# Kernel tuning notes

Measured on AMD Instinct MI355X. Metric: run time of the kernel, lower is better.

Reference implementation:

```python
import math
import jax, jax.numpy as jnp
import numpy as np

NUM_HEADS = 16
HEAD_DIM = 128
BLOCK = 256
EPS = 1e-6


def _get_slopes(n):
    def p2(n):
        start = 2 ** (-2 ** (-(math.log2(n) - 3)))
        return [start * start ** i for i in range(n)]
    if math.log2(n).is_integer():
        return p2(n)
    c = 2 ** math.floor(math.log2(n))
    return p2(c) + _get_slopes(2 * c)[0::2][: n - c]


def setup_inputs() -> dict:
    key = jax.random.key(0)
    ks = jax.random.split(key, 4)
    d_in, d_out = 2048, 2048
    x = jax.random.normal(ks[0], (2, 4096, d_in), dtype=jnp.float32)
    Wqkv = jax.random.normal(ks[1], (d_in, 3 * NUM_HEADS * HEAD_DIM), dtype=jnp.float32) * 0.02
    Wg = jax.random.normal(ks[2], (d_in, NUM_HEADS * HEAD_DIM), dtype=jnp.float32) * 0.02
    Wout = jax.random.normal(ks[3], (NUM_HEADS * HEAD_DIM, d_out), dtype=jnp.float32) * 0.02
    norm_w = jnp.ones((NUM_HEADS * HEAD_DIM,), dtype=jnp.float32)
    return {"x": x, "Wqkv": Wqkv, "Wg": Wg, "Wout": Wout, "norm_w": norm_w}


def reference(x, Wqkv, Wg, Wout, norm_w):
    b, n, _ = x.shape
    h, d = NUM_HEADS, HEAD_DIM
    nb = n // BLOCK  # seq_len chosen divisible by block_size

    # slopes (ALiBi-style), shape [h,1,1]
    slope = jnp.asarray(_get_slopes(h), dtype=jnp.float32).reshape(h, 1, 1)

    qkv = jax.nn.silu(x @ Wqkv)                       # [b,n,3hd]
    qkv = qkv.reshape(b, n, h, 3 * d)
    q, k, v = jnp.split(qkv, 3, axis=-1)              # each [b,n,h,d]
    q = q.transpose(0, 2, 1, 3)                       # [b,h,n,d]
    k = k.transpose(0, 2, 1, 3)
    v = v.transpose(0, 2, 1, 3)

    # per-position decay factors within a block
    arr = jnp.arange(BLOCK, dtype=jnp.float32) + 1.0          # [B]
    q_decay = jnp.exp(-slope * arr[:, None])                  # [h,B,1]
    k_decay = jnp.exp(-slope * (BLOCK - arr[:, None]))        # [h,B,1]
    idx = arr[:, None] - arr[None, :]                         # [B,B]
    diag_decay = jnp.where(idx >= 0, jnp.exp(-slope[None] * idx[None, None]), 0.0)  # [1,h,B,B]
    block_decay = jnp.exp(-slope * BLOCK)                     # [h,1,1]

    # blocked xs: [nb, b, h, B, d]
    def to_blocks(t):
        return t.reshape(b, h, nb, BLOCK, d).transpose(2, 0, 1, 3, 4)

    qb, kb, vb = to_blocks(q), to_blocks(k), to_blocks(v)

    def step(kv, blk):
        qi, ki, vi = blk                                       # [b,h,B,d]
        # inter-block: (qi * q_decay) @ kv  -> [b,h,B,d]
        non_diag = jnp.einsum('bhmd,bhde->bhme', qi * q_decay, kv)
        # intra-block causal decayed attention
        qk = jnp.einsum('bhmd,bhnd->bhmn', qi, ki) * diag_decay
        diag = jnp.einsum('bhmn,bhne->bhme', qk, vi)
        out = non_diag + diag
        kv_new = block_decay * kv + jnp.einsum('bhmd,bhme->bhde', ki * k_decay, vi)
        return kv_new, out

    kv0 = jnp.zeros((b, h, d, d), dtype=jnp.float32)
    _, out_blocks = jax.lax.scan(step, kv0, (qb, kb, vb))      # [nb,b,h,B,d]
    o = out_blocks.transpose(1, 2, 0, 3, 4).reshape(b, h, n, d)
    o = o.transpose(0, 2, 1, 3).reshape(b, n, h * d)           # [b,n,hd]

    # T5 (RMS) LayerNorm
    var = jnp.mean(o * o, axis=-1, keepdims=True)
    o = o * jax.lax.rsqrt(var + EPS) * norm_w

    # output gate and projection
    o = jax.nn.sigmoid(x @ Wg) * o
    return o @ Wout
```

## Files before the change

### kernel.cpp

```cpp
#include <hip/hip_runtime.h>
#include <cstddef>

typedef float f32x4 __attribute__((ext_vector_type(4)));
typedef __bf16 bf16x8 __attribute__((ext_vector_type(8)));
typedef unsigned short u16x8 __attribute__((ext_vector_type(8)));
typedef unsigned short u16x4 __attribute__((ext_vector_type(4)));

constexpr int NB = 2, S = 4096, H = 16, D = 128;
constexpr int DIN = 2048, NQKV = 6144, HD = 2048;
constexpr int BLK = 256, NBL = 16;

constexpr size_t SZ_XB    = (size_t)NB * S * DIN * 2;
constexpr size_t SZ_WQKVT = (size_t)NQKV * DIN * 2;
constexpr size_t SZ_WGT   = (size_t)HD * DIN * 2;
constexpr size_t SZ_WOUTT = (size_t)HD * HD * 2;
constexpr size_t SZ_QKVB  = (size_t)NB * S * NQKV * 2;
constexpr size_t SZ_GB    = (size_t)NB * S * HD * 2;
constexpr size_t SZ_ST    = (size_t)NB * H * NBL * D * D * 2;
constexpr size_t SZ_OB    = (size_t)NB * S * HD * 2;

__device__ __forceinline__ float bf2f(unsigned short u) {
  return __uint_as_float(((unsigned)u) << 16);
}
__device__ __forceinline__ unsigned short f2bf(float f) {
  unsigned u = __float_as_uint(f);
  u += 0x7fffu + ((u >> 16) & 1u);
  return (unsigned short)(u >> 16);
}
__device__ __forceinline__ void gload16(const void* g, void* l) {
  __builtin_amdgcn_global_load_lds(
      (const __attribute__((address_space(1))) unsigned int*)g,
      (__attribute__((address_space(3))) unsigned int*)l, 16, 0, 0);
}

__global__ __launch_bounds__(256) void cvt_bf16(
    const float* __restrict__ in, unsigned short* __restrict__ out) {
  const size_t id = (size_t)blockIdx.x * 256 + threadIdx.x;
  const float4 a = *(const float4*)&in[id * 8];
  const float4 c = *(const float4*)&in[id * 8 + 4];
  u16x8 o;
  o[0] = f2bf(a.x); o[1] = f2bf(a.y); o[2] = f2bf(a.z); o[3] = f2bf(a.w);
  o[4] = f2bf(c.x); o[5] = f2bf(c.y); o[6] = f2bf(c.z); o[7] = f2bf(c.w);
  *(u16x8*)&out[id * 8] = o;
}

__global__ __launch_bounds__(256) void transpose_cvt(
    const float* __restrict__ W, unsigned short* __restrict__ Wt, int K, int N) {
  __shared__ unsigned short tile[32][33];
  const int n0 = blockIdx.x * 32, k0 = blockIdx.y * 32;
  const int t = threadIdx.x;
  const int r = t >> 3, c4 = (t & 7) * 4;
  const float4 v = *(const float4*)&W[(size_t)(k0 + r) * N + n0 + c4];
  tile[r][c4 + 0] = f2bf(v.x);
  tile[r][c4 + 1] = f2bf(v.y);
  tile[r][c4 + 2] = f2bf(v.z);
  tile[r][c4 + 3] = f2bf(v.w);
  __syncthreads();
  u16x4 o;
  #pragma unroll
  for (int i = 0; i < 4; ++i) o[i] = tile[c4 + i][r];
  *(u16x4*)&Wt[(size_t)(n0 + r) * K + k0 + c4] = o;
}

template<int ACT>
__global__ __launch_bounds__(256, 3) void gemm128(
    const unsigned short* __restrict__ A, const unsigned short* __restrict__ Bt,
    void* __restrict__ O1, void* __restrict__ O2,
    int M, int N, int K, int NSPLIT) {
  __shared__ unsigned short lds[16384];
  char* ldsb = (char*)lds;
  const int t = threadIdx.x;
  const int lane = t & 63, wave = t >> 6;
  const int wr = wave >> 1, wc = wave & 1;
  const int l15 = lane & 15;

  const int nbm = M >> 7;
  const int nbmx = nbm >> 3;
  const int xcd = blockIdx.x & 7, q = blockIdx.x >> 3;
  const int bm = xcd * nbmx + (q % nbmx);
  const int bn = q / nbmx;

  const int cg = (t & 7) ^ ((t >> 3) & 7);
  const unsigned short* sA = A  + (size_t)(bm * 128 + (t >> 3)) * K + cg * 8;
  const unsigned short* sB = Bt + (size_t)(bn * 128 + (t >> 3)) * K + cg * 8;
  const int dstb = t << 4;

  int offA[2][4], offB[2][4];
  #pragma unroll
  for (int kk = 0; kk < 2; ++kk) {
    #pragma unroll
    for (int m = 0; m < 4; ++m) {
      const int row = wr * 64 + m * 16 + l15;
      offA[kk][m] = row * 128 + (((kk * 4 + (lane >> 4)) ^ (row & 7)) << 4);
    }
    #pragma unroll
    for (int n = 0; n < 4; ++n) {
      const int row = wc * 64 + n * 16 + l15;
      offB[kk][n] = 16384 + row * 128 + (((kk * 4 + (lane >> 4)) ^ (row & 7)) << 4);
    }
  }

  const int NT = K >> 6;
  f32x4 acc[4][4] = {};
  for (int u = 0; u < NT; ++u) {
    __syncthreads();
    const int ko = u * 64;
    #pragma unroll
    for (int i = 0; i < 4; ++i) {
      gload16(sA + (size_t)(i * 32) * K + ko, ldsb + i * 4096 + dstb);
      gload16(sB + (size_t)(i * 32) * K + ko, ldsb + 16384 + i * 4096 + dstb);
    }
    asm volatile("s_waitcnt vmcnt(0)" ::: "memory");
    __syncthreads();
    #pragma unroll
    for (int kk = 0; kk < 2; ++kk) {
      bf16x8 af[4], bfr[4];
      #pragma unroll
      for (int m = 0; m < 4; ++m) af[m] = *(const bf16x8*)(ldsb + offA[kk][m]);
      #pragma unroll
      for (int n = 0; n < 4; ++n) bfr[n] = *(const bf16x8*)(ldsb + offB[kk][n]);
      #pragma unroll
      for (int m = 0; m < 4; ++m)
        #pragma unroll
        for (int n = 0; n < 4; ++n)
          acc[m][n] = __builtin_amdgcn_mfma_f32_16x16x32_bf16(af[m], bfr[n], acc[m][n], 0, 0, 0);
    }
  }

  const int ro = (lane >> 4) * 4, co = l15;
  const bool lo = (bn * 128) < NSPLIT;
  #pragma unroll
  for (int m = 0; m < 4; ++m)
    #pragma unroll
    for (int n = 0; n < 4; ++n) {
      const int gc = bn * 128 + wc * 64 + n * 16 + co;
      #pragma unroll
      for (int r = 0; r < 4; ++r) {
        const int gr = bm * 128 + wr * 64 + m * 16 + ro + r;
        float v = acc[m][n][r];
        if constexpr (ACT == 0) {
          ((float*)O1)[(size_t)gr * N + gc] = v;
        } else {
          if (lo) {
            v = v / (1.f + __expf(-v));
            ((unsigned short*)O1)[(size_t)gr * NSPLIT + gc] = f2bf(v);
          } else {
            v = 1.f / (1.f + __expf(-v));
            ((unsigned short*)O2)[(size_t)gr * (N - NSPLIT) + (gc - NSPLIT)] = f2bf(v);
          }
        }
      }
    }
}

__global__ __launch_bounds__(256) void kv_outer(
    const unsigned short* __restrict__ qkv, unsigned short* __restrict__ st) {
  const int gid = blockIdx.x;
  const int j = gid & 15;
  const int bh = gid >> 4;
  const int h = bh & 15;
  const int b = bh >> 4;
  const float slope = exp2f(-0.5f * (float)(h + 1));
  const int t = threadIdx.x;
  __shared__ unsigned short kl[64][136];
  __shared__ unsigned short vl[64][136];
  float acc[8][8] = {};
  const int e0 = (t >> 4) * 8, f0 = (t & 15) * 8;
  for (int ch = 0; ch < 4; ++ch) {
    if (ch) __syncthreads();
    #pragma unroll
    for (int i = 0; i < 4; ++i) {
      const int cc = t + 256 * i;
      const int r = cc >> 4, c0 = (cc & 15) * 8;
      const int mb = ch * 64 + r;
      const int seq = b * S + j * BLK + mb;
      const u16x8 k8 = *(const u16x8*)&qkv[(size_t)seq * NQKV + h * 384 + 128 + c0];
      const float kd = expf(-slope * (float)(255 - mb));
      u16x8 kw;
      #pragma unroll
      for (int q2 = 0; q2 < 8; ++q2) kw[q2] = f2bf(bf2f(k8[q2]) * kd);
      *(u16x8*)&kl[r][c0] = kw;
      *(u16x8*)&vl[r][c0] = *(const u16x8*)&qkv[(size_t)seq * NQKV + h * 384 + 256 + c0];
    }
    __syncthreads();
    for (int m = 0; m < 64; ++m) {
      const u16x8 k8 = *(const u16x8*)&kl[m][e0];
      const u16x8 v8 = *(const u16x8*)&vl[m][f0];
      float kf[8], vf[8];
      #pragma unroll
      for (int q2 = 0; q2 < 8; ++q2) { kf[q2] = bf2f(k8[q2]); vf[q2] = bf2f(v8[q2]); }
      #pragma unroll
      for (int i = 0; i < 8; ++i)
        #pragma unroll
        for (int q2 = 0; q2 < 8; ++q2) acc[i][q2] += kf[i] * vf[q2];
    }
  }
  const size_t base = (size_t)gid * (D * D);
  #pragma unroll
  for (int q2 = 0; q2 < 8; ++q2) {
    u16x8 ow;
    #pragma unroll
    for (int i = 0; i < 8; ++i) ow[i] = f2bf(acc[i][q2]);
    *(u16x8*)&st[base + (size_t)(f0 + q2) * D + e0] = ow;
  }
}

__global__ __launch_bounds__(256) void kv_scan(unsigned short* __restrict__ st) {
  const int id = blockIdx.x * 256 + threadIdx.x;
  const int ef = id & (D * D - 1);
  const int bh = id >> 14;
  const int h = bh & 15;
  const float slope = exp2f(-0.5f * (float)(h + 1));
  const float bd = expf(-slope * 256.f);
  unsigned short* p = st + (size_t)bh * NBL * D * D + ef;
  float cur = 0.f;
  #pragma unroll
  for (int jj = 0; jj < NBL; ++jj) {
    const float m = bf2f(p[(size_t)jj * D * D]);
    p[(size_t)jj * D * D] = f2bf(cur);
    cur = bd * cur + m;
  }
}

__global__ __launch_bounds__(256) void attn_mfma(
    const unsigned short* __restrict__ qkv, const unsigned short* __restrict__ st,
    unsigned short* __restrict__ ob) {
  const int gid = blockIdx.x;
  const int half = gid & 1;
  const int rest = gid >> 1;
  const int j = rest & 15;
  const int bh = rest >> 4;
  const int h = bh & 15;
  const int b = bh >> 4;
  const float slope = exp2f(-0.5f * (float)(h + 1));
  const int t = threadIdx.x;
  const int lane = t & 63, wave = t >> 6, wr = wave >> 1, wc = wave & 1;

  __shared__ unsigned short ql[128][136];
  __shared__ unsigned short cb[128][136];
  __shared__ unsigned short pl[128][136];

  {
    const int r = t >> 4, c0 = (t & 15) * 8;
    const size_t stbase = (size_t)rest * (D * D);
    #pragma unroll
    for (int p = 0; p < 8; ++p) {
      const int seq = b * S + j * BLK + half * 128 + r + p * 16;
      *(u16x8*)&ql[r + p * 16][c0] = *(const u16x8*)&qkv[(size_t)seq * NQKV + h * 384 + c0];
      *(u16x8*)&cb[r + p * 16][c0] = *(const u16x8*)&st[stbase + (size_t)(r + p * 16) * D + c0];
    }
  }
  __syncthreads();

  f32x4 acc[4][4] = {};
  #pragma unroll
  for (int kk = 0; kk < 4; ++kk) {
    bf16x8 af[4], bfr[4];
    #pragma unroll
    for (int m = 0; m < 4; ++m)
      af[m] = *(const bf16x8*)&ql[wr * 64 + m * 16 + (lane & 15)][kk * 32 + (lane >> 4) * 8];
    #pragma unroll
    for (int n = 0; n < 4; ++n)
      bfr[n] = *(const bf16x8*)&cb[wc * 64 + n * 16 + (lane & 15)][kk * 32 + (lane >> 4) * 8];
    #pragma unroll
    for (int m = 0; m < 4; ++m)
      #pragma unroll
      for (int n = 0; n < 4; ++n)
        acc[m][n] = __builtin_amdgcn_mfma_f32_16x16x32_bf16(af[m], bfr[n], acc[m][n], 0, 0, 0);
  }
  const int ro = (lane >> 4) * 4;
  #pragma unroll
  for (int m = 0; m < 4; ++m)
    #pragma unroll
    for (int r = 0; r < 4; ++r) {
      const int gm = half * 128 + wr * 64 + m * 16 + ro + r;
      const float qd = expf(-slope * (float)(gm + 1));
      #pragma unroll
      for (int n = 0; n < 4; ++n) acc[m][n][r] *= qd;
    }

  const int nch = 1 + half;
  for (int c = 0; c < nch; ++c) {
    __syncthreads();
    {
      const int r = t >> 4, c0 = (t & 15) * 8;
      #pragma unroll
      for (int p = 0; p < 8; ++p) {
        const int seq = b * S + j * BLK + c * 128 + r + p * 16;
        *(u16x8*)&cb[r + p * 16][c0] = *(const u16x8*)&qkv[(size_t)seq * NQKV + h * 384 + 128 + c0];
      }
    }
    __syncthreads();
    f32x4 sacc[4][4] = {};
    #pragma unroll
    for (int kk = 0; kk < 4; ++kk) {
      bf16x8 af[4], bfr[4];
      #pragma unroll
      for (int m = 0; m < 4; ++m)
        af[m] = *(const bf16x8*)&ql[wr * 64 + m * 16 + (lane & 15)][kk * 32 + (lane >> 4) * 8];
      #pragma unroll
      for (int n = 0; n < 4; ++n)
        bfr[n] = *(const bf16x8*)&cb[wc * 64 + n * 16 + (lane & 15)][kk * 32 + (lane >> 4) * 8];
      #pragma unroll
      for (int m = 0; m < 4; ++m)
        #pragma unroll
        for (int n = 0; n < 4; ++n)
          sacc[m][n] = __builtin_amdgcn_mfma_f32_16x16x32_bf16(af[m], bfr[n], sacc[m][n], 0, 0, 0);
    }
    #pragma unroll
    for (int m = 0; m < 4; ++m)
      #pragma unroll
      for (int n = 0; n < 4; ++n) {
        const int lc = wc * 64 + n * 16 + (lane & 15);
        const int gp = c * 128 + lc;
        #pragma unroll
        for (int r = 0; r < 4; ++r) {
          const int lm = wr * 64 + m * 16 + ro + r;
          const int gm = half * 128 + lm;
          const float dd = (gm >= gp) ? expf(-slope * (float)(gm - gp)) : 0.f;
          pl[lm][lc] = f2bf(sacc[m][n][r] * dd);
        }
      }
    __syncthreads();
    {
      const int vr = t & 15, vc0 = (t >> 4) * 8;
      #pragma unroll
      for (int p = 0; p < 8; ++p) {
        const int row = vr + p * 16;
        const int seq = b * S + j * BLK + c * 128 + row;
        const u16x8 vv = *(const u16x8*)&qkv[(size_t)seq * NQKV + h * 384 + 256 + vc0];
        #pragma unroll
        for (int i = 0; i < 8; ++i) cb[vc0 + i][row] = vv[i];
      }
    }
    __syncthreads();
    #pragma unroll
    for (int kk = 0; kk < 4; ++kk) {
      bf16x8 af[4], bfr[4];
      #pragma unroll
      for (int m = 0; m < 4; ++m)
        af[m] = *(const bf16x8*)&pl[wr * 64 + m * 16 + (lane & 15)][kk * 32 + (lane >> 4) * 8];
      #pragma unroll
      for (int n = 0; n < 4; ++n)
        bfr[n] = *(const bf16x8*)&cb[wc * 64 + n * 16 + (lane & 15)][kk * 32 + (lane >> 4) * 8];
      #pragma unroll
      for (int m = 0; m < 4; ++m)
        #pragma unroll
        for (int n = 0; n < 4; ++n)
          acc[m][n] = __builtin_amdgcn_mfma_f32_16x16x32_bf16(af[m], bfr[n], acc[m][n], 0, 0, 0);
    }
  }

  #pragma unroll
  for (int m = 0; m < 4; ++m)
    #pragma unroll
    for (int n = 0; n < 4; ++n) {
      const int fc = h * D + wc * 64 + n * 16 + (lane & 15);
      #pragma unroll
      for (int r = 0; r < 4; ++r) {
        const int seq = b * S + j * BLK + half * 128 + wr * 64 + m * 16 + ro + r;
        ob[(size_t)seq * HD + fc] = f2bf(acc[m][n][r]);
      }
    }
}

__global__ __launch_bounds__(256) void norm_gate(
    const unsigned short* __restrict__ ob, const unsigned short* __restrict__ gb,
    const float* __restrict__ nw, unsigned short* __restrict__ og) {
  const int row = blockIdx.x;
  const int t = threadIdx.x;
  const u16x8 ov = *(const u16x8*)&ob[(size_t)row * HD + t * 8];
  float f[8];
  float ss = 0.f;
  #pragma unroll
  for (int i = 0; i < 8; ++i) { f[i] = bf2f(ov[i]); ss += f[i] * f[i]; }
  #pragma unroll
  for (int off = 32; off > 0; off >>= 1) ss += __shfl_down(ss, off, 64);
  __shared__ float red[4];
  if ((t & 63) == 0) red[t >> 6] = ss;
  __syncthreads();
  const float rms = rsqrtf((red[0] + red[1] + red[2] + red[3]) * (1.f / HD) + 1e-6f);
  const u16x8 gv = *(const u16x8*)&gb[(size_t)row * HD + t * 8];
  u16x8 ow;
  #pragma unroll
  for (int i = 0; i < 8; ++i)
    ow[i] = f2bf(f[i] * rms * nw[t * 8 + i] * bf2f(gv[i]));
  *(u16x8*)&og[(size_t)row * HD + t * 8] = ow;
}

extern "C" void kernel_launch(void* const* d_in, const int* in_sizes, int n_in,
                              void* d_out, int out_size, void* d_ws, size_t ws_size,
                              hipStream_t stream) {
  (void)in_sizes; (void)n_in; (void)out_size; (void)ws_size;
  const float* x    = (const float*)d_in[0];
  const float* Wqkv = (const float*)d_in[1];
  const float* Wg   = (const float*)d_in[2];
  const float* Wout = (const float*)d_in[3];
  const float* nw   = (const float*)d_in[4];

  char* ws = (char*)d_ws;
  unsigned short* xb    = (unsigned short*)ws; ws += SZ_XB;
  unsigned short* wqkvt = (unsigned short*)ws; ws += SZ_WQKVT;
  unsigned short* wgt   = (unsigned short*)ws; ws += SZ_WGT;
  unsigned short* woutt = (unsigned short*)ws; ws += SZ_WOUTT;
  unsigned short* qkvb  = (unsigned short*)ws; ws += SZ_QKVB;
  unsigned short* gb    = (unsigned short*)ws; ws += SZ_GB;
  unsigned short* st    = (unsigned short*)ws; ws += SZ_ST;
  unsigned short* ob    = (unsigned short*)ws; ws += SZ_OB;
  unsigned short* og    = xb;
  (void)wgt;

  cvt_bf16<<<dim3((NB * S * DIN) / (256 * 8)), 256, 0, stream>>>(x, xb);
  transpose_cvt<<<dim3(NQKV / 32, DIN / 32), 256, 0, stream>>>(Wqkv, wqkvt, DIN, NQKV);
  transpose_cvt<<<dim3(HD / 32, DIN / 32), 256, 0, stream>>>(Wg, wgt, DIN, HD);
  transpose_cvt<<<dim3(HD / 32, HD / 32), 256, 0, stream>>>(Wout, woutt, HD, HD);

  gemm128<3><<<dim3((NB * S / 128) * ((NQKV + HD) / 128)), 256, 0, stream>>>(
      xb, wqkvt, qkvb, gb, NB * S, NQKV + HD, DIN, NQKV);

  kv_outer<<<dim3(NB * H * NBL), 256, 0, stream>>>(qkvb, st);
  kv_scan<<<dim3((NB * H * D * D) / 256), 256, 0, stream>>>(st);
  attn_mfma<<<dim3(NB * H * NBL * 2), 256, 0, stream>>>(qkvb, st, ob);

  norm_gate<<<dim3(NB * S), 256, 0, stream>>>(ob, gb, nw, og);
  gemm128<0><<<dim3((NB * S / 128) * (HD / 128)), 256, 0, stream>>>(
      og, woutt, d_out, nullptr, NB * S, HD, HD, 0);
}
```

Before: 524.0 us.

## Use MFMA for per-block KV outer products and keep Q fragments in registers

The kv_outer kernel switches from scalar FMA outer products to bf16 MFMA. It stages transposed K (scaled by its decay) and V tiles in shared memory so each wave computes a 64x64 tile of the 128x128 state. In attn_mfma, the Q fragments are loaded from global memory straight into registers once and reused across all three matmuls, which drops the Q shared-memory tile and raises occupancy to two blocks per CU via launch bounds. The trade-offs are more register pressure, scattered 2-byte transposed writes to shared memory and to the state output, and bf16 rounding of products inside the MFMA path.

```diff
diff --git a/kernel.cpp b/kernel.cpp
--- a/kernel.cpp
+++ b/kernel.cpp
@@ -162,47 +162,59 @@
   const int b = bh >> 4;
   const float slope = exp2f(-0.5f * (float)(h + 1));
   const int t = threadIdx.x;
-  __shared__ unsigned short kl[64][136];
-  __shared__ unsigned short vl[64][136];
-  float acc[8][8] = {};
-  const int e0 = (t >> 4) * 8, f0 = (t & 15) * 8;
+  const int lane = t & 63, wave = t >> 6, wr = wave >> 1, wc = wave & 1;
+  const int l15 = lane & 15;
+  __shared__ unsigned short vt[128][72];
+  __shared__ unsigned short kt[128][72];
+  f32x4 acc[4][4] = {};
+  const int mm = t & 63;
+  const int c0 = (t >> 6) * 32;
   for (int ch = 0; ch < 4; ++ch) {
     if (ch) __syncthreads();
+    const int m = ch * 64 + mm;
+    const int seq = b * S + j * BLK + m;
+    const float kd = expf(-slope * (float)(255 - m));
+    const unsigned short* row = &qkv[(size_t)seq * NQKV + h * 384];
     #pragma unroll
     for (int i = 0; i < 4; ++i) {
-      const int cc = t + 256 * i;
-      const int r = cc >> 4, c0 = (cc & 15) * 8;
-      const int mb = ch * 64 + r;
-      const int seq = b * S + j * BLK + mb;
-      const u16x8 k8 = *(const u16x8*)&qkv[(size_t)seq * NQKV + h * 384 + 128 + c0];
-      const float kd = expf(-slope * (float)(255 - mb));
-      u16x8 kw;
-      #pragma unroll
-      for (int q2 = 0; q2 < 8; ++q2) kw[q2] = f2bf(bf2f(k8[q2]) * kd);
-      *(u16x8*)&kl[r][c0] = kw;
-      *(u16x8*)&vl[r][c0] = *(const u16x8*)&qkv[(size_t)seq * NQKV + h * 384 + 256 + c0];
-    }
-    __syncthreads();
-    for (int m = 0; m < 64; ++m) {
-      const u16x8 k8 = *(const u16x8*)&kl[m][e0];
-      const u16x8 v8 = *(const u16x8*)&vl[m][f0];
-      float kf[8], vf[8];
-      #pragma unroll
-      for (int q2 = 0; q2 < 8; ++q2) { kf[q2] = bf2f(k8[q2]); vf[q2] = bf2f(v8[q2]); }
-      #pragma unroll
-      for (int i = 0; i < 8; ++i)
-        #pragma unroll
-        for (int q2 = 0; q2 < 8; ++q2) acc[i][q2] += kf[i] * vf[q2];
+      const u16x8 k8 = *(const u16x8*)&row[128 + c0 + i * 8];
+      const u16x8 v8 = *(const u16x8*)&row[256 + c0 + i * 8];
+      #pragma unroll
+      for (int q2 = 0; q2 < 8; ++q2) {
+        kt[c0 + i * 8 + q2][mm] = f2bf(bf2f(k8[q2]) * kd);
+        vt[c0 + i * 8 + q2][mm] = v8[q2];
+      }
+    }
+    __syncthreads();
+    #pragma unroll
+    for (int kk = 0; kk < 2; ++kk) {
+      bf16x8 af[4], bfr[4];
+      #pragma unroll
+      for (int mi = 0; mi < 4; ++mi)
+        af[mi] = *(const bf16x8*)&vt[wr * 64 + mi * 16 + l15][kk * 32 + (lane >> 4) * 8];
+      #pragma unroll
+      for (int n = 0; n < 4; ++n)
+        bfr[n] = *(const bf16x8*)&kt[wc * 64 + n * 16 + l15][kk * 32 + (lane >> 4) * 8];
+      #pragma unroll
+      for (int mi = 0; mi < 4; ++mi)
+        #pragma unroll
+        for (int n = 0; n < 4; ++n)
+          acc[mi][n] = __builtin_amdgcn_mfma_f32_16x16x32_bf16(af[mi], bfr[n], acc[mi][n], 0, 0, 0);
     }
   }
   const size_t base = (size_t)gid * (D * D);
-  #pragma unroll
-  for (int q2 = 0; q2 < 8; ++q2) {
-    u16x8 ow;
-    #pragma unroll
-    for (int i = 0; i < 8; ++i) ow[i] = f2bf(acc[i][q2]);
-    *(u16x8*)&st[base + (size_t)(f0 + q2) * D + e0] = ow;
-  }
+  const int ro = (lane >> 4) * 4;
+  #pragma unroll
+  for (int mi = 0; mi < 4; ++mi)
+    #pragma unroll
+    for (int n = 0; n < 4; ++n) {
+      const int e = wc * 64 + n * 16 + l15;
+      #pragma unroll
+      for (int r = 0; r < 4; ++r) {
+        const int f = wr * 64 + mi * 16 + ro + r;
+        st[base + (size_t)f * D + e] = f2bf(acc[mi][n][r]);
+      }
+    }
 }
 
 __global__ __launch_bounds__(256) void kv_scan(unsigned short* __restrict__ st) {
@@ -222,7 +234,7 @@
   }
 }
 
-__global__ __launch_bounds__(256) void attn_mfma(
+__global__ __launch_bounds__(256, 2) void attn_mfma(
     const unsigned short* __restrict__ qkv, const unsigned short* __restrict__ st,
     unsigned short* __restrict__ ob) {
   const int gid = blockIdx.x;
@@ -236,29 +248,31 @@
   const int t = threadIdx.x;
   const int lane = t & 63, wave = t >> 6, wr = wave >> 1, wc = wave & 1;
 
-  __shared__ unsigned short ql[128][136];
   __shared__ unsigned short cb[128][136];
   __shared__ unsigned short pl[128][136];
 
+  bf16x8 af[4][4];
+  #pragma unroll
+  for (int m = 0; m < 4; ++m) {
+    const int seq = b * S + j * BLK + half * 128 + wr * 64 + m * 16 + (lane & 15);
+    const unsigned short* qrow = &qkv[(size_t)seq * NQKV + h * 384];
+    #pragma unroll
+    for (int kk = 0; kk < 4; ++kk)
+      af[kk][m] = *(const bf16x8*)&qrow[kk * 32 + (lane >> 4) * 8];
+  }
   {
     const int r = t >> 4, c0 = (t & 15) * 8;
     const size_t stbase = (size_t)rest * (D * D);
     #pragma unroll
-    for (int p = 0; p < 8; ++p) {
-      const int seq = b * S + j * BLK + half * 128 + r + p * 16;
-      *(u16x8*)&ql[r + p * 16][c0] = *(const u16x8*)&qkv[(size_t)seq * NQKV + h * 384 + c0];
+    for (int p = 0; p < 8; ++p)
       *(u16x8*)&cb[r + p * 16][c0] = *(const u16x8*)&st[stbase + (size_t)(r + p * 16) * D + c0];
-    }
   }
   __syncthreads();
 
   f32x4 acc[4][4] = {};
   #pragma unroll
   for (int kk = 0; kk < 4; ++kk) {
-    bf16x8 af[4], bfr[4];
-    #pragma unroll
-    for (int m = 0; m < 4; ++m)
-      af[m] = *(const bf16x8*)&ql[wr * 64 + m * 16 + (lane & 15)][kk * 32 + (lane >> 4) * 8];
+    bf16x8 bfr[4];
     #pragma unroll
     for (int n = 0; n < 4; ++n)
       bfr[n] = *(const bf16x8*)&cb[wc * 64 + n * 16 + (lane & 15)][kk * 32 + (lane >> 4) * 8];
@@ -266,7 +280,7 @@
     for (int m = 0; m < 4; ++m)
       #pragma unroll
       for (int n = 0; n < 4; ++n)
-        acc[m][n] = __builtin_amdgcn_mfma_f32_16x16x32_bf16(af[m], bfr[n], acc[m][n], 0, 0, 0);
+        acc[m][n] = __builtin_amdgcn_mfma_f32_16x16x32_bf16(af[kk][m], bfr[n], acc[m][n], 0, 0, 0);
   }
   const int ro = (lane >> 4) * 4;
   #pragma unroll
@@ -294,10 +308,7 @@
     f32x4 sacc[4][4] = {};
     #pragma unroll
     for (int kk = 0; kk < 4; ++kk) {
-      bf16x8 af[4], bfr[4];
-      #pragma unroll
-      for (int m = 0; m < 4; ++m)
-        af[m] = *(const bf16x8*)&ql[wr * 64 + m * 16 + (lane & 15)][kk * 32 + (lane >> 4) * 8];
+      bf16x8 bfr[4];
       #pragma unroll
       for (int n = 0; n < 4; ++n)
         bfr[n] = *(const bf16x8*)&cb[wc * 64 + n * 16 + (lane & 15)][kk * 32 + (lane >> 4) * 8];
@@ -305,7 +316,7 @@
       for (int m = 0; m < 4; ++m)
         #pragma unroll
         for (int n = 0; n < 4; ++n)
-          sacc[m][n] = __builtin_amdgcn_mfma_f32_16x16x32_bf16(af[m], bfr[n], sacc[m][n], 0, 0, 0);
+          sacc[m][n] = __builtin_amdgcn_mfma_f32_16x16x32_bf16(af[kk][m], bfr[n], sacc[m][n], 0, 0, 0);
     }
     #pragma unroll
     for (int m = 0; m < 4; ++m)
@@ -336,10 +347,10 @@
     __syncthreads();
     #pragma unroll
     for (int kk = 0; kk < 4; ++kk) {
-      bf16x8 af[4], bfr[4];
+      bf16x8 pf[4], bfr[4];
       #pragma unroll
       for (int m = 0; m < 4; ++m)
-        af[m] = *(const bf16x8*)&pl[wr * 64 + m * 16 + (lane & 15)][kk * 32 + (lane >> 4) * 8];
+        pf[m] = *(const bf16x8*)&pl[wr * 64 + m * 16 + (lane & 15)][kk * 32 + (lane >> 4) * 8];
       #pragma unroll
       for (int n = 0; n < 4; ++n)
         bfr[n] = *(const bf16x8*)&cb[wc * 64 + n * 16 + (lane & 15)][kk * 32 + (lane >> 4) * 8];
@@ -347,7 +358,7 @@
       for (int m = 0; m < 4; ++m)
         #pragma unroll
         for (int n = 0; n < 4; ++n)
-          acc[m][n] = __builtin_amdgcn_mfma_f32_16x16x32_bf16(af[m], bfr[n], acc[m][n], 0, 0, 0);
+          acc[m][n] = __builtin_amdgcn_mfma_f32_16x16x32_bf16(pf[m], bfr[n], acc[m][n], 0, 0, 0);
     }
   }
 
```

New measurement: 479.2 us. 1.09x faster.
